# Optimization experiments

Measured on AMD Instinct MI355X. Metric: run time of the kernel, lower is better.

The kernel has to match this reference:

```python
import jax, jax.numpy as jnp
import numpy as np

N = 100_000
E = 1_250_000
D = 64
PAIRS = 3  # layer_num=3 -> 3 (SAGE, GIN) pairs
EPS = 1e-5


def _linear_init(key, fi, fo):
    lim = 1.0 / np.sqrt(fi)
    k1, k2 = jax.random.split(key)
    W = jax.random.uniform(k1, (fi, fo), minval=-lim, maxval=lim, dtype=jnp.float32)
    b = jax.random.uniform(k2, (fo,), minval=-lim, maxval=lim, dtype=jnp.float32)
    return W, b


def setup_inputs() -> dict:
    key = jax.random.key(0)
    ks = jax.random.split(key, 40)
    # graph
    src = jax.random.randint(ks[0], (E,), 0, N, dtype=jnp.int32)
    dst = jax.random.randint(ks[1], (E,), 0, N, dtype=jnp.int32)
    sign = (jax.random.randint(ks[2], (E,), 0, 2, dtype=jnp.int32) * 2 - 1)
    edge_index_s = jnp.stack([src, dst, sign], axis=1)  # [E,3]
    init_emb = jax.random.normal(ks[3], (N, D), dtype=jnp.float32)
    rate_b = jax.random.uniform(ks[4], (1,), dtype=jnp.float32)

    def stack_lin(kbase, fi, fo, n):
        Ws, bs = [], []
        for i in range(n):
            W, b = _linear_init(jax.random.fold_in(kbase, i), fi, fo)
            Ws.append(W); bs.append(b)
        return jnp.stack(Ws), jnp.stack(bs)

    sage_lin_W, sage_lin_b = stack_lin(ks[5], D, D, PAIRS)
    sage_norm_w = jnp.ones((PAIRS, D), jnp.float32)
    sage_norm_b = jnp.zeros((PAIRS, D), jnp.float32)
    rsW, rsB = stack_lin(ks[6], 1, D, PAIRS)   # rate_scale Linear(1,D)
    rbW, rbB = stack_lin(ks[7], 1, D, PAIRS)   # rate_bias Linear(1,D)
    sage_rs_w, sage_rs_b = rsW[:, 0, :], rsB   # [PAIRS,D]
    sage_rb_w, sage_rb_b = rbW[:, 0, :], rbB
    gin_W1, gin_b1 = stack_lin(ks[8], D, D, PAIRS)
    gin_W2, gin_b2 = stack_lin(ks[9], D, D, PAIRS)
    fuse_W, fuse_b = _linear_init(ks[10], 2 * PAIRS * D, D)
    ro_W1, ro_b1 = _linear_init(ks[11], D, 128)
    ro_W2, ro_b2 = _linear_init(ks[12], 128, 128)
    ro_W3, ro_b3 = _linear_init(ks[13], 128, 1)
    ro_ln1_g = jnp.ones((128,), jnp.float32); ro_ln1_b = jnp.zeros((128,), jnp.float32)
    ro_ln2_g = jnp.ones((128,), jnp.float32); ro_ln2_b = jnp.zeros((128,), jnp.float32)
    return dict(init_emb=init_emb, edge_index_s=edge_index_s, rate_b=rate_b,
                sage_lin_W=sage_lin_W, sage_lin_b=sage_lin_b,
                sage_norm_w=sage_norm_w, sage_norm_b=sage_norm_b,
                sage_rs_w=sage_rs_w, sage_rs_b=sage_rs_b,
                sage_rb_w=sage_rb_w, sage_rb_b=sage_rb_b,
                gin_W1=gin_W1, gin_b1=gin_b1, gin_W2=gin_W2, gin_b2=gin_b2,
                fuse_W=fuse_W, fuse_b=fuse_b,
                ro_W1=ro_W1, ro_b1=ro_b1, ro_ln1_g=ro_ln1_g, ro_ln1_b=ro_ln1_b,
                ro_W2=ro_W2, ro_b2=ro_b2, ro_ln2_g=ro_ln2_g, ro_ln2_b=ro_ln2_b,
                ro_W3=ro_W3, ro_b3=ro_b3)


def _graph_norm(x, w, b, rs_w, rs_b, rb_w, rb_b, rate):
    # batch stats over nodes (dim 0), biased variance
    mean = x.mean(0, keepdims=True)
    var = x.var(0, keepdims=True)
    x_norm = (x - mean) / jnp.sqrt(var + EPS)
    gamma = w + (rs_w * rate + rs_b)  # rate_scale(rate_b)
    beta = b + (rb_w * rate + rb_b)
    return x_norm * gamma + beta


def _layer_norm(v, g, b):
    m = v.mean(-1, keepdims=True)
    va = v.var(-1, keepdims=True)
    return (v - m) / jnp.sqrt(va + EPS) * g + b


def _forward(init_emb, edge_index_s, rate_b,
             sage_lin_W, sage_lin_b, sage_norm_w, sage_norm_b,
             sage_rs_w, sage_rs_b, sage_rb_w, sage_rb_b,
             gin_W1, gin_b1, gin_W2, gin_b2,
             fuse_W, fuse_b,
             ro_W1, ro_b1, ro_ln1_g, ro_ln1_b,
             ro_W2, ro_b2, ro_ln2_g, ro_ln2_b,
             ro_W3, ro_b3):
    n = init_emb.shape[0]
    src = edge_index_s[:, 0]
    dst = edge_index_s[:, 1]
    sign = edge_index_s[:, 2].astype(init_emb.dtype)
    rate = rate_b.reshape(())
    # degree including self-loop (for mean aggregation with fill_value=1 self loops)
    deg = jax.ops.segment_sum(jnp.ones_like(sign), dst, num_segments=n) + 1.0  # [n]
    gelu = lambda t: jax.nn.gelu(t, approximate=False)  # torch nn.GELU default = exact

    x = init_emb
    outputs = []
    for i in range(PAIRS):
        # --- StableEfficientEdgeSAGEConv (mean aggr, sign-scaled, self-loops, skip=Identity) ---
        xt = x @ sage_lin_W[i] + sage_lin_b[i]
        msg = sign[:, None] * xt[src]                                   # gather + sign scale
        agg = (jax.ops.segment_sum(msg, dst, num_segments=n) + xt) / deg[:, None]
        h = agg + x                                                     # skip (in==out -> Identity)
        h = _graph_norm(h, sage_norm_w[i], sage_norm_b[i],
                        sage_rs_w[i], sage_rs_b[i], sage_rb_w[i], sage_rb_b[i], rate)
        x = gelu(h)                                                     # dropout: eval mode (no-op)
        outputs.append(x)
        # --- GINConv (sum aggr, eps=0, no self-loops) mlp = Lin-GELU-Lin ---
        agg2 = jax.ops.segment_sum(x[src], dst, num_segments=n)
        z = x + agg2
        x = gelu(z @ gin_W1[i] + gin_b1[i]) @ gin_W2[i] + gin_b2[i]
        outputs.append(x)

    x_dense = jnp.concatenate(outputs, axis=1)          # [n, 6*D]
    x_final = x_dense @ fuse_W + fuse_b                 # [n, D]
    # readout MLP (2 hidden layers + head), eval-mode dropout
    hdd = jax.nn.relu(_layer_norm(x_final @ ro_W1 + ro_b1, ro_ln1_g, ro_ln1_b))
    hdd = jax.nn.relu(_layer_norm(hdd @ ro_W2 + ro_b2, ro_ln2_g, ro_ln2_b))
    prob = jax.nn.sigmoid(hdd @ ro_W3 + ro_b3)          # [n, 1]
    return x_final, prob


def reference(init_emb, edge_index_s, rate_b,
              sage_lin_W, sage_lin_b, sage_norm_w, sage_norm_b,
              sage_rs_w, sage_rs_b, sage_rb_w, sage_rb_b,
              gin_W1, gin_b1, gin_W2, gin_b2,
              fuse_W, fuse_b,
              ro_W1, ro_b1, ro_ln1_g, ro_ln1_b,
              ro_W2, ro_b2, ro_ln2_g, ro_ln2_b,
              ro_W3, ro_b3):
    return _forward(init_emb, edge_index_s, rate_b,
                    sage_lin_W, sage_lin_b, sage_norm_w, sage_norm_b,
                    sage_rs_w, sage_rs_b, sage_rb_w, sage_rb_b,
                    gin_W1, gin_b1, gin_W2, gin_b2,
                    fuse_W, fuse_b,
                    ro_W1, ro_b1, ro_ln1_g, ro_ln1_b,
                    ro_W2, ro_b2, ro_ln2_g, ro_ln2_b,
                    ro_W3, ro_b3)
```

## Files before the change

kernel.cpp:

```cpp
#include <hip/hip_runtime.h>
#include <hip/hip_bf16.h>
#include <math.h>


#define NBSHIFT 9
#define NBSIZE  512

__device__ __forceinline__ float gelu_f(float x) {
    return 0.5f * x * (1.0f + erff(x * 0.70710678118654752440f));
}
__device__ __forceinline__ unsigned short f2bf(float x) {
    __hip_bfloat16 h = __float2bfloat16(x);
    return *reinterpret_cast<unsigned short*>(&h);
}
__device__ __forceinline__ unsigned pack2bf(float a, float b) {
    return (unsigned)f2bf(a) | ((unsigned)f2bf(b) << 16);
}
__device__ __forceinline__ float bf2f(unsigned short u) {
    return __uint_as_float((unsigned)u << 16);
}

__global__ __launch_bounds__(256) void gemm64(
    const float* __restrict__ A,
    const float* __restrict__ Wa, const float* __restrict__ ba,
    unsigned short* __restrict__ Cb, int n)
{
    __shared__ __align__(16) float At[64][68];
    __shared__ __align__(16) float Ws[64][68];
    const int tid = threadIdx.x;
    const int tx = tid & 15, ty = tid >> 4;
    const int rowBase = blockIdx.x * 64;

    #pragma unroll
    for (int i = 0; i < 4; ++i) {
        int v  = tid + i * 256;
        int r  = v >> 4;
        int k4 = (v & 15) * 4;
        float4 a = make_float4(0.f, 0.f, 0.f, 0.f);
        int grow = rowBase + r;
        if (grow < n) a = *(const float4*)(A + (size_t)grow * 64 + k4);
        At[k4 + 0][r] = a.x; At[k4 + 1][r] = a.y;
        At[k4 + 2][r] = a.z; At[k4 + 3][r] = a.w;
        *(float4*)&Ws[r][k4] = *(const float4*)(Wa + r * 64 + k4);
    }
    __syncthreads();

    const int r0 = ty * 4, c0 = tx * 4;
    float acc[4][4];
    #pragma unroll
    for (int j = 0; j < 4; ++j) {
        float bv = ba[c0 + j];
        #pragma unroll
        for (int i = 0; i < 4; ++i) acc[i][j] = bv;
    }
    #pragma unroll 16
    for (int k = 0; k < 64; ++k) {
        float4 av = *(const float4*)&At[k][r0];
        float4 wv = *(const float4*)&Ws[k][c0];
        float a4[4] = {av.x, av.y, av.z, av.w};
        float w4[4] = {wv.x, wv.y, wv.z, wv.w};
        #pragma unroll
        for (int i = 0; i < 4; ++i)
            #pragma unroll
            for (int j = 0; j < 4; ++j)
                acc[i][j] = fmaf(a4[i], w4[j], acc[i][j]);
    }
    #pragma unroll
    for (int i = 0; i < 4; ++i) {
        int grow = rowBase + r0 + i;
        if (grow < n) {
            uint2 u;
            u.x = pack2bf(acc[i][0], acc[i][1]);
            u.y = pack2bf(acc[i][2], acc[i][3]);
            *(uint2*)(Cb + (size_t)grow * 64 + c0) = u;
        }
    }
}

template<bool FIRST>
__global__ __launch_bounds__(256) void act_fuse(
    const float* __restrict__ h,
    const float* __restrict__ colsum, const float* __restrict__ colsumsq,
    const float* __restrict__ nw, const float* __restrict__ nb,
    const float* __restrict__ rsw, const float* __restrict__ rsb,
    const float* __restrict__ rbw, const float* __restrict__ rbb,
    const float* __restrict__ rate_p, float inv_n,
    const float* __restrict__ Wf, const float* __restrict__ bf,
    unsigned short* __restrict__ xb, float* __restrict__ xfinal, int n)
{
    __shared__ __align__(16) float At[64][68];
    __shared__ __align__(16) float Ws[64][68];
    __shared__ float ab_s[128];
    const int tid = threadIdx.x;
    const int tx = tid & 15, ty = tid >> 4;
    const int rowBase = blockIdx.x * 64;

    if (tid < 64) {
        float mean = colsum[tid] * inv_n;
        float var  = colsumsq[tid] * inv_n - mean * mean;
        float rstd = rsqrtf(var + 1e-5f);
        float rate = rate_p[0];
        float gamma = nw[tid] + (rsw[tid] * rate + rsb[tid]);
        float beta  = nb[tid] + (rbw[tid] * rate + rbb[tid]);
        float a = rstd * gamma;
        ab_s[tid] = a;
        ab_s[64 + tid] = beta - mean * a;
    }
    __syncthreads();

    #pragma unroll
    for (int i = 0; i < 4; ++i) {
        int v  = tid + i * 256;
        int r  = v >> 4;
        int k4 = (v & 15) * 4;
        int grow = rowBase + r;
        float4 a = make_float4(0.f, 0.f, 0.f, 0.f);
        if (grow < n) {
            float4 hv = *(const float4*)(h + (size_t)grow * 64 + k4);
            a.x = gelu_f(fmaf(hv.x, ab_s[k4 + 0], ab_s[64 + k4 + 0]));
            a.y = gelu_f(fmaf(hv.y, ab_s[k4 + 1], ab_s[64 + k4 + 1]));
            a.z = gelu_f(fmaf(hv.z, ab_s[k4 + 2], ab_s[64 + k4 + 2]));
            a.w = gelu_f(fmaf(hv.w, ab_s[k4 + 3], ab_s[64 + k4 + 3]));
            uint2 u;
            u.x = pack2bf(a.x, a.y);
            u.y = pack2bf(a.z, a.w);
            *(uint2*)(xb + (size_t)grow * 64 + k4) = u;
        }
        At[k4 + 0][r] = a.x; At[k4 + 1][r] = a.y;
        At[k4 + 2][r] = a.z; At[k4 + 3][r] = a.w;
        *(float4*)&Ws[r][k4] = *(const float4*)(Wf + r * 64 + k4);
    }
    __syncthreads();

    const int r0 = ty * 4, c0 = tx * 4;
    float acc[4][4];
    if (FIRST) {
        #pragma unroll
        for (int j = 0; j < 4; ++j) {
            float bv = bf[c0 + j];
            #pragma unroll
            for (int i = 0; i < 4; ++i) acc[i][j] = bv;
        }
    } else {
        #pragma unroll
        for (int i = 0; i < 4; ++i)
            #pragma unroll
            for (int j = 0; j < 4; ++j) acc[i][j] = 0.f;
    }
    #pragma unroll 16
    for (int k = 0; k < 64; ++k) {
        float4 av = *(const float4*)&At[k][r0];
        float4 wv = *(const float4*)&Ws[k][c0];
        float a4[4] = {av.x, av.y, av.z, av.w};
        float w4[4] = {wv.x, wv.y, wv.z, wv.w};
        #pragma unroll
        for (int i = 0; i < 4; ++i)
            #pragma unroll
            for (int j = 0; j < 4; ++j)
                acc[i][j] = fmaf(a4[i], w4[j], acc[i][j]);
    }
    #pragma unroll
    for (int i = 0; i < 4; ++i) {
        int grow = rowBase + r0 + i;
        if (grow < n) {
            float4 r = make_float4(acc[i][0], acc[i][1], acc[i][2], acc[i][3]);
            float* cp = xfinal + (size_t)grow * 64 + c0;
            if (!FIRST) {
                float4 c = *(const float4*)cp;
                r.x += c.x; r.y += c.y; r.z += c.z; r.w += c.w;
            }
            *(float4*)cp = r;
        }
    }
}

template<bool NEXT>
__global__ __launch_bounds__(256) void gin_fuse(
    const float* __restrict__ z,
    const float* __restrict__ W1, const float* __restrict__ b1,
    const float* __restrict__ W2, const float* __restrict__ b2,
    const float* __restrict__ Wf,
    const float* __restrict__ Wn, const float* __restrict__ bn,
    float* __restrict__ xout, float* __restrict__ xfinal,
    unsigned short* __restrict__ bfout, int n)
{
    __shared__ __align__(16) float At[64][68];
    __shared__ __align__(16) float Ws[64][68];
    const int tid = threadIdx.x;
    const int tx = tid & 15, ty = tid >> 4;
    const int rowBase = blockIdx.x * 64;
    const int r0 = ty * 4, c0 = tx * 4;

    #pragma unroll
    for (int i = 0; i < 4; ++i) {
        int v  = tid + i * 256;
        int r  = v >> 4;
        int k4 = (v & 15) * 4;
        float4 a = make_float4(0.f, 0.f, 0.f, 0.f);
        int grow = rowBase + r;
        if (grow < n) a = *(const float4*)(z + (size_t)grow * 64 + k4);
        At[k4 + 0][r] = a.x; At[k4 + 1][r] = a.y;
        At[k4 + 2][r] = a.z; At[k4 + 3][r] = a.w;
        *(float4*)&Ws[r][k4] = *(const float4*)(W1 + r * 64 + k4);
    }
    __syncthreads();

    float acc[4][4];
    #pragma unroll
    for (int j = 0; j < 4; ++j) {
        float bv = b1[c0 + j];
        #pragma unroll
        for (int i = 0; i < 4; ++i) acc[i][j] = bv;
    }
    #pragma unroll 16
    for (int k = 0; k < 64; ++k) {
        float4 av = *(const float4*)&At[k][r0];
        float4 wv = *(const float4*)&Ws[k][c0];
        float a4[4] = {av.x, av.y, av.z, av.w};
        float w4[4] = {wv.x, wv.y, wv.z, wv.w};
        #pragma unroll
        for (int i = 0; i < 4; ++i)
            #pragma unroll
            for (int j = 0; j < 4; ++j)
                acc[i][j] = fmaf(a4[i], w4[j], acc[i][j]);
    }

    __syncthreads();
    #pragma unroll
    for (int i = 0; i < 4; ++i)
        #pragma unroll
        for (int j = 0; j < 4; ++j)
            At[c0 + j][r0 + i] = gelu_f(acc[i][j]);
    #pragma unroll
    for (int i = 0; i < 4; ++i) {
        int v = tid + i * 256;
        int k = v >> 4, c4 = (v & 15) * 4;
        *(float4*)&Ws[k][c4] = *(const float4*)(W2 + k * 64 + c4);
    }
    __syncthreads();
    float acc2[4][4];
    #pragma unroll
    for (int j = 0; j < 4; ++j) {
        float bv = b2[c0 + j];
        #pragma unroll
        for (int i = 0; i < 4; ++i) acc2[i][j] = bv;
    }
    #pragma unroll 16
    for (int k = 0; k < 64; ++k) {
        float4 av = *(const float4*)&At[k][r0];
        float4 wv = *(const float4*)&Ws[k][c0];
        float a4[4] = {av.x, av.y, av.z, av.w};
        float w4[4] = {wv.x, wv.y, wv.z, wv.w};
        #pragma unroll
        for (int i = 0; i < 4; ++i)
            #pragma unroll
            for (int j = 0; j < 4; ++j)
                acc2[i][j] = fmaf(a4[i], w4[j], acc2[i][j]);
    }
    #pragma unroll
    for (int i = 0; i < 4; ++i) {
        int grow = rowBase + r0 + i;
        if (grow < n)
            *(float4*)(xout + (size_t)grow * 64 + c0) =
                make_float4(acc2[i][0], acc2[i][1], acc2[i][2], acc2[i][3]);
    }

    __syncthreads();
    #pragma unroll
    for (int i = 0; i < 4; ++i)
        #pragma unroll
        for (int j = 0; j < 4; ++j)
            At[c0 + j][r0 + i] = acc2[i][j];
    #pragma unroll
    for (int i = 0; i < 4; ++i) {
        int v = tid + i * 256;
        int k = v >> 4, c4 = (v & 15) * 4;
        *(float4*)&Ws[k][c4] = *(const float4*)(Wf + k * 64 + c4);
    }
    __syncthreads();
    float acc3[4][4];
    #pragma unroll
    for (int i = 0; i < 4; ++i)
        #pragma unroll
        for (int j = 0; j < 4; ++j) acc3[i][j] = 0.f;
    #pragma unroll 16
    for (int k = 0; k < 64; ++k) {
        float4 av = *(const float4*)&At[k][r0];
        float4 wv = *(const float4*)&Ws[k][c0];
        float a4[4] = {av.x, av.y, av.z, av.w};
        float w4[4] = {wv.x, wv.y, wv.z, wv.w};
        #pragma unroll
        for (int i = 0; i < 4; ++i)
            #pragma unroll
            for (int j = 0; j < 4; ++j)
                acc3[i][j] = fmaf(a4[i], w4[j], acc3[i][j]);
    }
    #pragma unroll
    for (int i = 0; i < 4; ++i) {
        int grow = rowBase + r0 + i;
        if (grow < n) {
            float* cp = xfinal + (size_t)grow * 64 + c0;
            float4 c = *(const float4*)cp;
            c.x += acc3[i][0]; c.y += acc3[i][1];
            c.z += acc3[i][2]; c.w += acc3[i][3];
            *(float4*)cp = c;
        }
    }

    if (NEXT) {
        __syncthreads();
        #pragma unroll
        for (int i = 0; i < 4; ++i) {
            int v = tid + i * 256;
            int k = v >> 4, c4 = (v & 15) * 4;
            *(float4*)&Ws[k][c4] = *(const float4*)(Wn + k * 64 + c4);
        }
        __syncthreads();
        float acc4[4][4];
        #pragma unroll
        for (int j = 0; j < 4; ++j) {
            float bv = bn[c0 + j];
            #pragma unroll
            for (int i = 0; i < 4; ++i) acc4[i][j] = bv;
        }
        #pragma unroll 16
        for (int k = 0; k < 64; ++k) {
            float4 av = *(const float4*)&At[k][r0];
            float4 wv = *(const float4*)&Ws[k][c0];
            float a4[4] = {av.x, av.y, av.z, av.w};
            float w4[4] = {wv.x, wv.y, wv.z, wv.w};
            #pragma unroll
            for (int i = 0; i < 4; ++i)
                #pragma unroll
                for (int j = 0; j < 4; ++j)
                    acc4[i][j] = fmaf(a4[i], w4[j], acc4[i][j]);
        }
        #pragma unroll
        for (int i = 0; i < 4; ++i) {
            int grow = rowBase + r0 + i;
            if (grow < n) {
                uint2 u;
                u.x = pack2bf(acc4[i][0], acc4[i][1]);
                u.y = pack2bf(acc4[i][2], acc4[i][3]);
                *(uint2*)(bfout + (size_t)grow * 64 + c0) = u;
            }
        }
    }
}

__global__ void init_buckets(int* __restrict__ bucket_cursor, int Bn, int cap) {
    int t = threadIdx.x;
    if (t < Bn) bucket_cursor[t] = t * cap;
}

__global__ __launch_bounds__(256) void bucketA(
    const int* __restrict__ eidx, int* __restrict__ bucket_cursor,
    uint2* __restrict__ inter, int E)
{
    __shared__ int cnt[256], lo[256], cur[256], garr[256];
    __shared__ int tot_s;
    __shared__ uint2 stage[4096];
    const int tid = threadIdx.x;
    cnt[tid] = 0;
    __syncthreads();

    const int base = blockIdx.x * 4096;
    int pay[16], dfull[16];
    #pragma unroll
    for (int i = 0; i < 16; ++i) {
        int e = base + i * 256 + tid;
        dfull[i] = -1;
        if (e < E) {
            int s  = __builtin_nontemporal_load(eidx + e * 3 + 0);
            int d  = __builtin_nontemporal_load(eidx + e * 3 + 1);
            int sg = __builtin_nontemporal_load(eidx + e * 3 + 2);
            if (sg < 0) s |= 0x80000000;
            pay[i] = s;
            dfull[i] = d;
            atomicAdd(&cnt[d >> NBSHIFT], 1);
        }
    }
    __syncthreads();

    lo[tid] = cnt[tid];
    __syncthreads();
    for (int off = 1; off < 256; off <<= 1) {
        int t = (tid >= off) ? lo[tid - off] : 0;
        __syncthreads();
        lo[tid] += t;
        __syncthreads();
    }
    if (tid == 255) tot_s = lo[255];
    int excl = lo[tid] - cnt[tid];
    __syncthreads();
    lo[tid] = excl;
    cur[tid] = 0;
    if (cnt[tid] > 0) garr[tid] = atomicAdd(bucket_cursor + tid, cnt[tid]);
    __syncthreads();

    #pragma unroll
    for (int i = 0; i < 16; ++i) {
        if (dfull[i] >= 0) {
            int k = dfull[i] >> NBSHIFT;
            int r = atomicAdd(&cur[k], 1);
            stage[lo[k] + r] = make_uint2((unsigned)pay[i], (unsigned)dfull[i]);
        }
    }
    __syncthreads();

    const int tot = tot_s;
    for (int i = tid; i < tot; i += 256) {
        uint2 en = stage[i];
        int k = (int)(en.y >> NBSHIFT);
        inter[garr[k] + (i - lo[k])] = en;
    }
}

__global__ __launch_bounds__(256) void bucketB1(
    const uint2* __restrict__ inter, const int* __restrict__ bucket_cursor,
    int* __restrict__ deg_i, int cap, int n)
{
    __shared__ int cnt[NBSIZE];
    const int b = blockIdx.x, tid = threadIdx.x;
    cnt[tid] = 0; cnt[tid + 256] = 0;
    __syncthreads();
    const int base = b * cap;
    const int len = bucket_cursor[b] - base;
    for (int i = tid; i < len; i += 256)
        atomicAdd(&cnt[inter[base + i].y & (NBSIZE - 1)], 1);
    __syncthreads();
    const int nb0 = b << NBSHIFT;
    if (nb0 + tid < n)       deg_i[nb0 + tid]       = cnt[tid];
    if (nb0 + 256 + tid < n) deg_i[nb0 + 256 + tid] = cnt[256 + tid];
}

__global__ __launch_bounds__(256) void bucketB2(
    const uint2* __restrict__ inter, const int* __restrict__ bucket_cursor,
    const int* __restrict__ row_ptr, int* __restrict__ payload, int cap, int n)
{
    __shared__ int cur[NBSIZE];
    const int b = blockIdx.x, tid = threadIdx.x;
    const int nb0 = b << NBSHIFT;
    cur[tid]       = (nb0 + tid < n)       ? row_ptr[nb0 + tid]       : 0;
    cur[tid + 256] = (nb0 + 256 + tid < n) ? row_ptr[nb0 + 256 + tid] : 0;
    __syncthreads();
    const int base = b * cap;
    const int len = bucket_cursor[b] - base;
    for (int i = tid; i < len; i += 256) {
        uint2 en = inter[base + i];
        int pos = atomicAdd(&cur[en.y & (NBSIZE - 1)], 1);
        payload[pos] = (int)en.x;
    }
}

__global__ __launch_bounds__(256) void scan1(
    const int* __restrict__ deg_i, int* __restrict__ blocksum, int n, int chunk)
{
    int b = blockIdx.x;
    int lo = b * chunk, hi = min(lo + chunk, n);
    int s = 0;
    for (int i = lo + (int)threadIdx.x; i < hi; i += 256) s += deg_i[i];
    #pragma unroll
    for (int off = 32; off; off >>= 1) s += __shfl_xor(s, off, 64);
    __shared__ int ws[4];
    if ((threadIdx.x & 63) == 0) ws[threadIdx.x >> 6] = s;
    __syncthreads();
    if (threadIdx.x == 0) blocksum[b] = ws[0] + ws[1] + ws[2] + ws[3];
}

__global__ __launch_bounds__(256) void scan2(
    const int* __restrict__ blocksum, int* __restrict__ blockoff,
    int* __restrict__ row_ptr_n)
{
    int tid = threadIdx.x, lane = tid & 63, wid = tid >> 6;
    int orig = blocksum[tid];
    int v = orig;
    #pragma unroll
    for (int off = 1; off < 64; off <<= 1) {
        int t = __shfl_up(v, off, 64);
        if (lane >= off) v += t;
    }
    __shared__ int wt[4];
    if (lane == 63) wt[wid] = v;
    __syncthreads();
    int woff = 0;
    for (int w = 0; w < wid; ++w) woff += wt[w];
    blockoff[tid] = woff + v - orig;
    if (tid == 255) *row_ptr_n = woff + v;
}

__global__ __launch_bounds__(256) void scan3(
    const int* __restrict__ deg_i, const int* __restrict__ blockoff,
    int* __restrict__ row_ptr, float* __restrict__ rdeg, int n, int chunk)
{
    int b = blockIdx.x;
    int lo = b * chunk, hi = min(lo + chunk, n);
    int carry = blockoff[b];
    int tid = threadIdx.x, lane = tid & 63, wid = tid >> 6;
    __shared__ int wt[4];
    for (int base = lo; base < hi; base += 256) {
        int i = base + tid;
        int orig = (i < hi) ? deg_i[i] : 0;
        int v = orig;
        #pragma unroll
        for (int off = 1; off < 64; off <<= 1) {
            int t = __shfl_up(v, off, 64);
            if (lane >= off) v += t;
        }
        if (lane == 63) wt[wid] = v;
        __syncthreads();
        int woff = 0;
        for (int w = 0; w < wid; ++w) woff += wt[w];
        int tot = wt[0] + wt[1] + wt[2] + wt[3];
        int excl = carry + woff + (v - orig);
        if (i < hi) {
            row_ptr[i] = excl;
            rdeg[i]    = 1.0f / ((float)orig + 1.0f);
        }
        carry += tot;
        __syncthreads();
    }
}

__device__ __forceinline__ void accum8(float* a, uint4 u, float s) {
    a[0] = fmaf(__uint_as_float(u.x << 16),          s, a[0]);
    a[1] = fmaf(__uint_as_float(u.x & 0xffff0000u),  s, a[1]);
    a[2] = fmaf(__uint_as_float(u.y << 16),          s, a[2]);
    a[3] = fmaf(__uint_as_float(u.y & 0xffff0000u),  s, a[3]);
    a[4] = fmaf(__uint_as_float(u.z << 16),          s, a[4]);
    a[5] = fmaf(__uint_as_float(u.z & 0xffff0000u),  s, a[5]);
    a[6] = fmaf(__uint_as_float(u.w << 16),          s, a[6]);
    a[7] = fmaf(__uint_as_float(u.w & 0xffff0000u),  s, a[7]);
}

template<bool SAGE>
__global__ __launch_bounds__(256) void gather64(
    const int* __restrict__ row_ptr, const int* __restrict__ payload,
    const unsigned short* __restrict__ valb, const float* __restrict__ xprev,
    const float* __restrict__ rdeg, float* __restrict__ out,
    float* __restrict__ colsum, float* __restrict__ colsumsq, int n)
{
    const int tid  = threadIdx.x;
    const int lane = tid & 63;
    const int j8   = lane & 7;
    const int c0   = j8 * 8;
    const int wid  = tid >> 6;
    const int gg0  = (blockIdx.x * 256 + tid) >> 3;
    const int ng   = (gridDim.x * 256) >> 3;

    float st[8], st2[8];
    if (SAGE) {
        #pragma unroll
        for (int k = 0; k < 8; ++k) { st[k] = 0.f; st2[k] = 0.f; }
    }

    for (int node = gg0; __any(node < n); node += ng) {
        const bool active  = node < n;
        const int  selfrow = active ? node : 0;
        const int  beg     = active ? row_ptr[node]     : 0;
        const int  end     = active ? row_ptr[node + 1] : 0;

        int t = (end - beg + 3) >> 2;
        t = max(t, __shfl_xor(t, 8, 64));
        t = max(t, __shfl_xor(t, 16, 64));
        t = max(t, __shfl_xor(t, 32, 64));

        float a[8];
        #pragma unroll
        for (int k = 0; k < 8; ++k) a[k] = 0.f;

        int p0 = (beg + 0 < end) ? payload[beg + 0] : 0;
        int p1 = (beg + 1 < end) ? payload[beg + 1] : 0;
        int p2 = (beg + 2 < end) ? payload[beg + 2] : 0;
        int p3 = (beg + 3 < end) ? payload[beg + 3] : 0;

        for (int it = 0; it < t; ++it) {
            const int i0 = beg + (it << 2);
            const bool w0 = i0 + 0 < end, w1 = i0 + 1 < end;
            const bool w2 = i0 + 2 < end, w3 = i0 + 3 < end;
            const int q0 = p0, q1 = p1, q2 = p2, q3 = p3;

            const int r0 = w0 ? (q0 & 0x7fffffff) : selfrow;
            const int r1 = w1 ? (q1 & 0x7fffffff) : selfrow;
            const int r2 = w2 ? (q2 & 0x7fffffff) : selfrow;
            const int r3 = w3 ? (q3 & 0x7fffffff) : selfrow;
            uint4 u0 = *(const uint4*)(valb + (size_t)r0 * 64 + c0);
            uint4 u1 = *(const uint4*)(valb + (size_t)r1 * 64 + c0);
            uint4 u2 = *(const uint4*)(valb + (size_t)r2 * 64 + c0);
            uint4 u3 = *(const uint4*)(valb + (size_t)r3 * 64 + c0);

            const int nb = i0 + 4;
            p0 = (nb + 0 < end) ? payload[nb + 0] : 0;
            p1 = (nb + 1 < end) ? payload[nb + 1] : 0;
            p2 = (nb + 2 < end) ? payload[nb + 2] : 0;
            p3 = (nb + 3 < end) ? payload[nb + 3] : 0;

            const float s0 = w0 ? ((SAGE && q0 < 0) ? -1.f : 1.f) : 0.f;
            const float s1 = w1 ? ((SAGE && q1 < 0) ? -1.f : 1.f) : 0.f;
            const float s2 = w2 ? ((SAGE && q2 < 0) ? -1.f : 1.f) : 0.f;
            const float s3 = w3 ? ((SAGE && q3 < 0) ? -1.f : 1.f) : 0.f;
            accum8(a, u0, s0);
            accum8(a, u1, s1);
            accum8(a, u2, s2);
            accum8(a, u3, s3);
        }

        uint4 us = *(const uint4*)(valb + (size_t)selfrow * 64 + c0);
        accum8(a, us, 1.f);

        if (SAGE) {
            const float rd = active ? rdeg[node] : 0.f;
            float4 xp0 = *(const float4*)(xprev + (size_t)selfrow * 64 + c0);
            float4 xp1 = *(const float4*)(xprev + (size_t)selfrow * 64 + c0 + 4);
            float xp[8] = {xp0.x, xp0.y, xp0.z, xp0.w,
                           xp1.x, xp1.y, xp1.z, xp1.w};
            float h[8];
            #pragma unroll
            for (int k = 0; k < 8; ++k) h[k] = fmaf(a[k], rd, xp[k]);
            if (active) {
                #pragma unroll
                for (int k = 0; k < 8; ++k) {
                    st[k]  += h[k];
                    st2[k] += h[k] * h[k];
                }
                *(float4*)(out + (size_t)node * 64 + c0) =
                    make_float4(h[0], h[1], h[2], h[3]);
                *(float4*)(out + (size_t)node * 64 + c0 + 4) =
                    make_float4(h[4], h[5], h[6], h[7]);
            }
        } else {
            if (active) {
                *(float4*)(out + (size_t)node * 64 + c0) =
                    make_float4(a[0], a[1], a[2], a[3]);
                *(float4*)(out + (size_t)node * 64 + c0 + 4) =
                    make_float4(a[4], a[5], a[6], a[7]);
            }
        }
    }

    if (SAGE) {
        #pragma unroll
        for (int k = 0; k < 8; ++k) {
            st[k]  += __shfl_xor(st[k], 8, 64);
            st[k]  += __shfl_xor(st[k], 16, 64);
            st[k]  += __shfl_xor(st[k], 32, 64);
            st2[k] += __shfl_xor(st2[k], 8, 64);
            st2[k] += __shfl_xor(st2[k], 16, 64);
            st2[k] += __shfl_xor(st2[k], 32, 64);
        }
        __shared__ float sh[2][4][64];
        if (lane < 8) {
            #pragma unroll
            for (int k = 0; k < 8; ++k) {
                sh[0][wid][c0 + k] = st[k];
                sh[1][wid][c0 + k] = st2[k];
            }
        }
        __syncthreads();
        if (tid < 64) {
            float a_ = sh[0][0][tid] + sh[0][1][tid] + sh[0][2][tid] + sh[0][3][tid];
            float b_ = sh[1][0][tid] + sh[1][1][tid] + sh[1][2][tid] + sh[1][3][tid];
            atomicAdd(colsum + tid, a_);
            atomicAdd(colsumsq + tid, b_);
        }
    }
}

__global__ __launch_bounds__(256) void readout1(
    const float* __restrict__ xf, const float* __restrict__ W1,
    const float* __restrict__ b1, const float* __restrict__ g1,
    const float* __restrict__ bt1, float* __restrict__ H, int n)
{
    __shared__ __align__(16) float At[64][68];
    __shared__ __align__(16) float Ws[64][132];
    const int tid = threadIdx.x;
    const int tx = tid & 15, ty = tid >> 4;
    const int rowBase = blockIdx.x * 64;

    #pragma unroll
    for (int i = 0; i < 4; ++i) {
        int v = tid + i * 256;
        int r = v >> 4, k4 = (v & 15) * 4;
        float4 a = make_float4(0.f, 0.f, 0.f, 0.f);
        int grow = rowBase + r;
        if (grow < n) a = *(const float4*)(xf + (size_t)grow * 64 + k4);
        At[k4 + 0][r] = a.x; At[k4 + 1][r] = a.y;
        At[k4 + 2][r] = a.z; At[k4 + 3][r] = a.w;
    }
    #pragma unroll
    for (int i = 0; i < 8; ++i) {
        int v = tid + i * 256;
        int k = v >> 5, c4 = (v & 31) * 4;
        *(float4*)&Ws[k][c4] = *(const float4*)(W1 + k * 128 + c4);
    }
    __syncthreads();

    const int r0 = ty * 4, c0 = tx * 8;
    float acc[4][8];
    #pragma unroll
    for (int j = 0; j < 8; ++j) {
        float bv = b1[c0 + j];
        #pragma unroll
        for (int i = 0; i < 4; ++i) acc[i][j] = bv;
    }
    #pragma unroll 8
    for (int k = 0; k < 64; ++k) {
        float4 av = *(const float4*)&At[k][r0];
        float4 w0 = *(const float4*)&Ws[k][c0];
        float4 w1v = *(const float4*)&Ws[k][c0 + 4];
        float a4[4] = {av.x, av.y, av.z, av.w};
        float w8[8] = {w0.x, w0.y, w0.z, w0.w, w1v.x, w1v.y, w1v.z, w1v.w};
        #pragma unroll
        for (int i = 0; i < 4; ++i)
            #pragma unroll
            for (int j = 0; j < 8; ++j)
                acc[i][j] = fmaf(a4[i], w8[j], acc[i][j]);
    }

    float gj[8], bj[8];
    #pragma unroll
    for (int j = 0; j < 8; ++j) { gj[j] = g1[c0 + j]; bj[j] = bt1[c0 + j]; }
    #pragma unroll
    for (int i = 0; i < 4; ++i) {
        int grow = rowBase + r0 + i;
        float s = 0.f, s2 = 0.f;
        #pragma unroll
        for (int j = 0; j < 8; ++j) { s += acc[i][j]; s2 += acc[i][j] * acc[i][j]; }
        #pragma unroll
        for (int off = 8; off; off >>= 1) {
            s  += __shfl_xor(s, off, 16);
            s2 += __shfl_xor(s2, off, 16);
        }
        float mean = s * (1.f / 128.f);
        float var  = s2 * (1.f / 128.f) - mean * mean;
        float rstd = rsqrtf(var + 1e-5f);
        float o[8];
        #pragma unroll
        for (int j = 0; j < 8; ++j)
            o[j] = fmaxf(fmaf((acc[i][j] - mean) * rstd, gj[j], bj[j]), 0.f);
        if (grow < n) {
            *(float4*)(H + (size_t)grow * 128 + c0)     = make_float4(o[0], o[1], o[2], o[3]);
            *(float4*)(H + (size_t)grow * 128 + c0 + 4) = make_float4(o[4], o[5], o[6], o[7]);
        }
    }
}

__global__ __launch_bounds__(256) void readout2(
    const float* __restrict__ H, const float* __restrict__ W2,
    const float* __restrict__ b2, const float* __restrict__ g2,
    const float* __restrict__ bt2, const float* __restrict__ W3,
    const float* __restrict__ b3, float* __restrict__ prob, int n)
{
    __shared__ __align__(16) float Ht[64][68];
    __shared__ __align__(16) float Ws[64][132];
    const int tid = threadIdx.x;
    const int tx = tid & 15, ty = tid >> 4;
    const int rowBase = blockIdx.x * 64;
    const int r0 = ty * 4, c0 = tx * 8;

    float acc[4][8];
    #pragma unroll
    for (int j = 0; j < 8; ++j) {
        float bv = b2[c0 + j];
        #pragma unroll
        for (int i = 0; i < 4; ++i) acc[i][j] = bv;
    }

    for (int kc = 0; kc < 2; ++kc) {
        if (kc) __syncthreads();
        #pragma unroll
        for (int i = 0; i < 4; ++i) {
            int v = tid + i * 256;
            int r = v >> 4, k4 = (v & 15) * 4;
            float4 a = make_float4(0.f, 0.f, 0.f, 0.f);
            int grow = rowBase + r;
            if (grow < n) a = *(const float4*)(H + (size_t)grow * 128 + kc * 64 + k4);
            Ht[k4 + 0][r] = a.x; Ht[k4 + 1][r] = a.y;
            Ht[k4 + 2][r] = a.z; Ht[k4 + 3][r] = a.w;
        }
        #pragma unroll
        for (int i = 0; i < 8; ++i) {
            int v = tid + i * 256;
            int k = v >> 5, c4 = (v & 31) * 4;
            *(float4*)&Ws[k][c4] = *(const float4*)(W2 + (kc * 64 + k) * 128 + c4);
        }
        __syncthreads();
        #pragma unroll 8
        for (int k = 0; k < 64; ++k) {
            float4 av = *(const float4*)&Ht[k][r0];
            float4 w0 = *(const float4*)&Ws[k][c0];
            float4 w1v = *(const float4*)&Ws[k][c0 + 4];
            float a4[4] = {av.x, av.y, av.z, av.w};
            float w8[8] = {w0.x, w0.y, w0.z, w0.w, w1v.x, w1v.y, w1v.z, w1v.w};
            #pragma unroll
            for (int i = 0; i < 4; ++i)
                #pragma unroll
                for (int j = 0; j < 8; ++j)
                    acc[i][j] = fmaf(a4[i], w8[j], acc[i][j]);
        }
    }

    float gj[8], bj[8], w3[8];
    #pragma unroll
    for (int j = 0; j < 8; ++j) {
        gj[j] = g2[c0 + j]; bj[j] = bt2[c0 + j]; w3[j] = W3[c0 + j];
    }
    const float bias3 = b3[0];
    #pragma unroll
    for (int i = 0; i < 4; ++i) {
        int grow = rowBase + r0 + i;
        float s = 0.f, s2 = 0.f;
        #pragma unroll
        for (int j = 0; j < 8; ++j) { s += acc[i][j]; s2 += acc[i][j] * acc[i][j]; }
        #pragma unroll
        for (int off = 8; off; off >>= 1) {
            s  += __shfl_xor(s, off, 16);
            s2 += __shfl_xor(s2, off, 16);
        }
        float mean = s * (1.f / 128.f);
        float var  = s2 * (1.f / 128.f) - mean * mean;
        float rstd = rsqrtf(var + 1e-5f);
        float d = 0.f;
        #pragma unroll
        for (int j = 0; j < 8; ++j) {
            float v = fmaxf(fmaf((acc[i][j] - mean) * rstd, gj[j], bj[j]), 0.f);
            d = fmaf(v, w3[j], d);
        }
        #pragma unroll
        for (int off = 8; off; off >>= 1) d += __shfl_xor(d, off, 16);
        if (tx == 0 && grow < n)
            prob[grow] = 1.f / (1.f + expf(-(d + bias3)));
    }
}

extern "C" void kernel_launch(void* const* d_in, const int* in_sizes, int n_in,
                              void* d_out, int out_size, void* d_ws, size_t ws_size,
                              hipStream_t stream)
{
    const float* init_emb = (const float*)d_in[0];
    const int*   eidx     = (const int*)d_in[1];
    const float* rate_b   = (const float*)d_in[2];
    const float* sage_W   = (const float*)d_in[3];
    const float* sage_b   = (const float*)d_in[4];
    const float* norm_w   = (const float*)d_in[5];
    const float* norm_b   = (const float*)d_in[6];
    const float* rs_w     = (const float*)d_in[7];
    const float* rs_b     = (const float*)d_in[8];
    const float* rb_w     = (const float*)d_in[9];
    const float* rb_b     = (const float*)d_in[10];
    const float* gin_W1   = (const float*)d_in[11];
    const float* gin_b1   = (const float*)d_in[12];
    const float* gin_W2   = (const float*)d_in[13];
    const float* gin_b2   = (const float*)d_in[14];
    const float* fuse_W   = (const float*)d_in[15];
    const float* fuse_b   = (const float*)d_in[16];
    const float* ro_W1    = (const float*)d_in[17];
    const float* ro_b1    = (const float*)d_in[18];
    const float* ln1_g    = (const float*)d_in[19];
    const float* ln1_b    = (const float*)d_in[20];
    const float* ro_W2    = (const float*)d_in[21];
    const float* ro_b2    = (const float*)d_in[22];
    const float* ln2_g    = (const float*)d_in[23];
    const float* ln2_b    = (const float*)d_in[24];
    const float* ro_W3    = (const float*)d_in[25];
    const float* ro_b3    = (const float*)d_in[26];

    const int N = in_sizes[0] / 64;
    const int E = in_sizes[1] / 3;
    const size_t nf = (size_t)N * 64;

    float* bufA  = (float*)d_ws;
    float* bufB  = bufA + nf;
    float* bufC  = bufB + nf;
    unsigned short* bfbuf = (unsigned short*)(bufC + nf);
    float* rdeg  = (float*)(bfbuf + nf);
    float* stats = rdeg + N;
    int*   row_ptr  = (int*)(stats + 3 * 256);
    int*   deg_i    = row_ptr + (N + 1);
    int*   blocksum = deg_i + N;
    int*   blockoff = blocksum + 256;
    int*   bucket_cursor = blockoff + 256;
    int*   payload  = bucket_cursor + 256;
    uint2* inter    = (uint2*)bufC;

    float* xfinal = (float*)d_out;
    float* prob   = xfinal + nf;
    float* H      = bufA;

    const int gemm_blocks = (N + 63) / 64;
    const int gather_blocks = 2048;
    const int chunk  = (N + 255) / 256;
    const float inv_n = 1.0f / (float)N;

    const int Bn   = (N + NBSIZE - 1) / NBSIZE;
    const int meanb = (E + Bn - 1) / Bn;
    const int cap  = meanb + meanb / 8 + 64;
    const int ablocks = (E + 4095) / 4096;

    hipMemsetAsync(stats, 0, 3 * 256 * sizeof(float), stream);
    init_buckets<<<1, 256, 0, stream>>>(bucket_cursor, Bn, cap);
    bucketA<<<ablocks, 256, 0, stream>>>(eidx, bucket_cursor, inter, E);
    bucketB1<<<Bn, 256, 0, stream>>>(inter, bucket_cursor, deg_i, cap, N);
    scan1<<<256, 256, 0, stream>>>(deg_i, blocksum, N, chunk);
    scan2<<<1, 256, 0, stream>>>(blocksum, blockoff, row_ptr + N);
    scan3<<<256, 256, 0, stream>>>(deg_i, blockoff, row_ptr, rdeg, N, chunk);
    bucketB2<<<Bn, 256, 0, stream>>>(inter, bucket_cursor, row_ptr, payload, cap, N);

    for (int p = 0; p < 3; ++p) {
        const float* Xp = (p == 0) ? init_emb : (p == 1 ? (const float*)bufB : (const float*)bufC);
        float* B2p = (p == 1) ? bufC : bufB;
        float* cs = stats + p * 256;

        if (p == 0)
            gemm64<<<gemm_blocks, 256, 0, stream>>>(
                Xp, sage_W, sage_b, bfbuf, N);
        gather64<true><<<gather_blocks, 256, 0, stream>>>(
            row_ptr, payload, bfbuf, Xp, rdeg, B2p, cs, cs + 64, N);
        if (p == 0)
            act_fuse<true><<<gemm_blocks, 256, 0, stream>>>(
                B2p, cs, cs + 64,
                norm_w + p * 64, norm_b + p * 64, rs_w + p * 64, rs_b + p * 64,
                rb_w + p * 64, rb_b + p * 64, rate_b, inv_n,
                fuse_W, fuse_b, bfbuf, xfinal, N);
        else
            act_fuse<false><<<gemm_blocks, 256, 0, stream>>>(
                B2p, cs, cs + 64,
                norm_w + p * 64, norm_b + p * 64, rs_w + p * 64, rs_b + p * 64,
                rb_w + p * 64, rb_b + p * 64, rate_b, inv_n,
                fuse_W + (2 * p) * 4096, nullptr, bfbuf, xfinal, N);
        gather64<false><<<gather_blocks, 256, 0, stream>>>(
            row_ptr, payload, bfbuf, nullptr, nullptr, B2p, nullptr, nullptr, N);
        if (p < 2)
            gin_fuse<true><<<gemm_blocks, 256, 0, stream>>>(
                B2p, gin_W1 + p * 4096, gin_b1 + p * 64,
                gin_W2 + p * 4096, gin_b2 + p * 64,
                fuse_W + (2 * p + 1) * 4096,
                sage_W + (p + 1) * 4096, sage_b + (p + 1) * 64,
                B2p, xfinal, bfbuf, N);
        else
            gin_fuse<false><<<gemm_blocks, 256, 0, stream>>>(
                B2p, gin_W1 + p * 4096, gin_b1 + p * 64,
                gin_W2 + p * 4096, gin_b2 + p * 64,
                fuse_W + (2 * p + 1) * 4096,
                nullptr, nullptr, B2p, xfinal, nullptr, N);
    }

    readout1<<<gemm_blocks, 256, 0, stream>>>(
        xfinal, ro_W1, ro_b1, ln1_g, ln1_b, H, N);
    readout2<<<gemm_blocks, 256, 0, stream>>>(
        H, ro_W2, ro_b2, ln2_g, ln2_b, ro_W3, ro_b3, prob, N);
}
```

Baseline: 822.7 us.

## Vectorize transposed LDS tile stores and use nontemporal loads/stores in gather

```diff
diff --git a/kernel.cpp b/kernel.cpp
--- a/kernel.cpp
+++ b/kernel.cpp
@@ -5,6 +5,8 @@
 
 #define NBSHIFT 9
 #define NBSIZE  512
+
+typedef float vf4 __attribute__((ext_vector_type(4)));
 
 __device__ __forceinline__ float gelu_f(float x) {
     return 0.5f * x * (1.0f + erff(x * 0.70710678118654752440f));
@@ -30,18 +32,30 @@
     const int tid = threadIdx.x;
     const int tx = tid & 15, ty = tid >> 4;
     const int rowBase = blockIdx.x * 64;
-
-    #pragma unroll
-    for (int i = 0; i < 4; ++i) {
-        int v  = tid + i * 256;
-        int r  = v >> 4;
-        int k4 = (v & 15) * 4;
-        float4 a = make_float4(0.f, 0.f, 0.f, 0.f);
-        int grow = rowBase + r;
-        if (grow < n) a = *(const float4*)(A + (size_t)grow * 64 + k4);
-        At[k4 + 0][r] = a.x; At[k4 + 1][r] = a.y;
-        At[k4 + 2][r] = a.z; At[k4 + 3][r] = a.w;
-        *(float4*)&Ws[r][k4] = *(const float4*)(Wa + r * 64 + k4);
+    const int ty4 = ty * 4;
+
+    {
+        float4 R[4];
+        #pragma unroll
+        for (int i = 0; i < 4; ++i) {
+            int grow = rowBase + ty4 + i;
+            R[i] = make_float4(0.f, 0.f, 0.f, 0.f);
+            if (grow < n) R[i] = *(const float4*)(A + (size_t)grow * 64 + tx * 4);
+        }
+        #pragma unroll
+        for (int j = 0; j < 4; ++j) {
+            float4 c = make_float4(((const float*)&R[0])[j],
+                                   ((const float*)&R[1])[j],
+                                   ((const float*)&R[2])[j],
+                                   ((const float*)&R[3])[j]);
+            *(float4*)&At[tx * 4 + j][ty4] = c;
+        }
+        #pragma unroll
+        for (int i = 0; i < 4; ++i) {
+            int v = tid + i * 256;
+            int r = v >> 4, k4 = (v & 15) * 4;
+            *(float4*)&Ws[r][k4] = *(const float4*)(Wa + r * 64 + k4);
+        }
     }
     __syncthreads();
 
@@ -94,6 +108,7 @@
     const int tid = threadIdx.x;
     const int tx = tid & 15, ty = tid >> 4;
     const int rowBase = blockIdx.x * 64;
+    const int ty4 = ty * 4;
 
     if (tid < 64) {
         float mean = colsum[tid] * inv_n;
@@ -108,27 +123,43 @@
     }
     __syncthreads();
 
-    #pragma unroll
-    for (int i = 0; i < 4; ++i) {
-        int v  = tid + i * 256;
-        int r  = v >> 4;
-        int k4 = (v & 15) * 4;
-        int grow = rowBase + r;
-        float4 a = make_float4(0.f, 0.f, 0.f, 0.f);
-        if (grow < n) {
-            float4 hv = *(const float4*)(h + (size_t)grow * 64 + k4);
-            a.x = gelu_f(fmaf(hv.x, ab_s[k4 + 0], ab_s[64 + k4 + 0]));
-            a.y = gelu_f(fmaf(hv.y, ab_s[k4 + 1], ab_s[64 + k4 + 1]));
-            a.z = gelu_f(fmaf(hv.z, ab_s[k4 + 2], ab_s[64 + k4 + 2]));
-            a.w = gelu_f(fmaf(hv.w, ab_s[k4 + 3], ab_s[64 + k4 + 3]));
-            uint2 u;
-            u.x = pack2bf(a.x, a.y);
-            u.y = pack2bf(a.z, a.w);
-            *(uint2*)(xb + (size_t)grow * 64 + k4) = u;
-        }
-        At[k4 + 0][r] = a.x; At[k4 + 1][r] = a.y;
-        At[k4 + 2][r] = a.z; At[k4 + 3][r] = a.w;
-        *(float4*)&Ws[r][k4] = *(const float4*)(Wf + r * 64 + k4);
+    {
+        const float s0 = ab_s[tx * 4 + 0], s1 = ab_s[tx * 4 + 1];
+        const float s2 = ab_s[tx * 4 + 2], s3 = ab_s[tx * 4 + 3];
+        const float o0 = ab_s[64 + tx * 4 + 0], o1 = ab_s[64 + tx * 4 + 1];
+        const float o2 = ab_s[64 + tx * 4 + 2], o3 = ab_s[64 + tx * 4 + 3];
+        float4 R[4];
+        #pragma unroll
+        for (int i = 0; i < 4; ++i) {
+            int grow = rowBase + ty4 + i;
+            float4 a = make_float4(0.f, 0.f, 0.f, 0.f);
+            if (grow < n) {
+                float4 hv = *(const float4*)(h + (size_t)grow * 64 + tx * 4);
+                a.x = gelu_f(fmaf(hv.x, s0, o0));
+                a.y = gelu_f(fmaf(hv.y, s1, o1));
+                a.z = gelu_f(fmaf(hv.z, s2, o2));
+                a.w = gelu_f(fmaf(hv.w, s3, o3));
+                uint2 u;
+                u.x = pack2bf(a.x, a.y);
+                u.y = pack2bf(a.z, a.w);
+                *(uint2*)(xb + (size_t)grow * 64 + tx * 4) = u;
+            }
+            R[i] = a;
+        }
+        #pragma unroll
+        for (int j = 0; j < 4; ++j) {
+            float4 c = make_float4(((const float*)&R[0])[j],
+                                   ((const float*)&R[1])[j],
+                                   ((const float*)&R[2])[j],
+                                   ((const float*)&R[3])[j]);
+            *(float4*)&At[tx * 4 + j][ty4] = c;
+        }
+        #pragma unroll
+        for (int i = 0; i < 4; ++i) {
+            int v = tid + i * 256;
+            int r = v >> 4, k4 = (v & 15) * 4;
+            *(float4*)&Ws[r][k4] = *(const float4*)(Wf + r * 64 + k4);
+        }
     }
     __syncthreads();
 
@@ -190,18 +221,30 @@
     const int tx = tid & 15, ty = tid >> 4;
     const int rowBase = blockIdx.x * 64;
     const int r0 = ty * 4, c0 = tx * 4;
-
-    #pragma unroll
-    for (int i = 0; i < 4; ++i) {
-        int v  = tid + i * 256;
-        int r  = v >> 4;
-        int k4 = (v & 15) * 4;
-        float4 a = make_float4(0.f, 0.f, 0.f, 0.f);
-        int grow = rowBase + r;
-        if (grow < n) a = *(const float4*)(z + (size_t)grow * 64 + k4);
-        At[k4 + 0][r] = a.x; At[k4 + 1][r] = a.y;
-        At[k4 + 2][r] = a.z; At[k4 + 3][r] = a.w;
-        *(float4*)&Ws[r][k4] = *(const float4*)(W1 + r * 64 + k4);
+    const int ty4 = ty * 4;
+
+    {
+        float4 R[4];
+        #pragma unroll
+        for (int i = 0; i < 4; ++i) {
+            int grow = rowBase + ty4 + i;
+            R[i] = make_float4(0.f, 0.f, 0.f, 0.f);
+            if (grow < n) R[i] = *(const float4*)(z + (size_t)grow * 64 + tx * 4);
+        }
+        #pragma unroll
+        for (int j = 0; j < 4; ++j) {
+            float4 c = make_float4(((const float*)&R[0])[j],
+                                   ((const float*)&R[1])[j],
+                                   ((const float*)&R[2])[j],
+                                   ((const float*)&R[3])[j]);
+            *(float4*)&At[tx * 4 + j][ty4] = c;
+        }
+        #pragma unroll
+        for (int i = 0; i < 4; ++i) {
+            int v = tid + i * 256;
+            int r = v >> 4, k4 = (v & 15) * 4;
+            *(float4*)&Ws[r][k4] = *(const float4*)(W1 + r * 64 + k4);
+        }
     }
     __syncthreads();
 
@@ -227,10 +270,11 @@
 
     __syncthreads();
     #pragma unroll
-    for (int i = 0; i < 4; ++i)
-        #pragma unroll
-        for (int j = 0; j < 4; ++j)
-            At[c0 + j][r0 + i] = gelu_f(acc[i][j]);
+    for (int j = 0; j < 4; ++j) {
+        float4 c = make_float4(gelu_f(acc[0][j]), gelu_f(acc[1][j]),
+                               gelu_f(acc[2][j]), gelu_f(acc[3][j]));
+        *(float4*)&At[c0 + j][r0] = c;
+    }
     #pragma unroll
     for (int i = 0; i < 4; ++i) {
         int v = tid + i * 256;
@@ -267,10 +311,10 @@
 
     __syncthreads();
     #pragma unroll
-    for (int i = 0; i < 4; ++i)
-        #pragma unroll
-        for (int j = 0; j < 4; ++j)
-            At[c0 + j][r0 + i] = acc2[i][j];
+    for (int j = 0; j < 4; ++j) {
+        float4 c = make_float4(acc2[0][j], acc2[1][j], acc2[2][j], acc2[3][j]);
+        *(float4*)&At[c0 + j][r0] = c;
+    }
     #pragma unroll
     for (int i = 0; i < 4; ++i) {
         int v = tid + i * 256;
@@ -569,10 +613,10 @@
         #pragma unroll
         for (int k = 0; k < 8; ++k) a[k] = 0.f;
 
-        int p0 = (beg + 0 < end) ? payload[beg + 0] : 0;
-        int p1 = (beg + 1 < end) ? payload[beg + 1] : 0;
-        int p2 = (beg + 2 < end) ? payload[beg + 2] : 0;
-        int p3 = (beg + 3 < end) ? payload[beg + 3] : 0;
+        int p0 = (beg + 0 < end) ? __builtin_nontemporal_load(payload + beg + 0) : 0;
+        int p1 = (beg + 1 < end) ? __builtin_nontemporal_load(payload + beg + 1) : 0;
+        int p2 = (beg + 2 < end) ? __builtin_nontemporal_load(payload + beg + 2) : 0;
+        int p3 = (beg + 3 < end) ? __builtin_nontemporal_load(payload + beg + 3) : 0;
 
         for (int it = 0; it < t; ++it) {
             const int i0 = beg + (it << 2);
@@ -590,10 +634,10 @@
             uint4 u3 = *(const uint4*)(valb + (size_t)r3 * 64 + c0);
 
             const int nb = i0 + 4;
-            p0 = (nb + 0 < end) ? payload[nb + 0] : 0;
-            p1 = (nb + 1 < end) ? payload[nb + 1] : 0;
-            p2 = (nb + 2 < end) ? payload[nb + 2] : 0;
-            p3 = (nb + 3 < end) ? payload[nb + 3] : 0;
+            p0 = (nb + 0 < end) ? __builtin_nontemporal_load(payload + nb + 0) : 0;
+            p1 = (nb + 1 < end) ? __builtin_nontemporal_load(payload + nb + 1) : 0;
+            p2 = (nb + 2 < end) ? __builtin_nontemporal_load(payload + nb + 2) : 0;
+            p3 = (nb + 3 < end) ? __builtin_nontemporal_load(payload + nb + 3) : 0;
 
             const float s0 = w0 ? ((SAGE && q0 < 0) ? -1.f : 1.f) : 0.f;
             const float s1 = w1 ? ((SAGE && q1 < 0) ? -1.f : 1.f) : 0.f;
@@ -609,9 +653,11 @@
         accum8(a, us, 1.f);
 
         if (SAGE) {
-            const float rd = active ? rdeg[node] : 0.f;
-            float4 xp0 = *(const float4*)(xprev + (size_t)selfrow * 64 + c0);
-            float4 xp1 = *(const float4*)(xprev + (size_t)selfrow * 64 + c0 + 4);
+            const float rd = active ? __builtin_nontemporal_load(rdeg + node) : 0.f;
+            vf4 xp0 = __builtin_nontemporal_load(
+                (const vf4*)(xprev + (size_t)selfrow * 64 + c0));
+            vf4 xp1 = __builtin_nontemporal_load(
+                (const vf4*)(xprev + (size_t)selfrow * 64 + c0 + 4));
             float xp[8] = {xp0.x, xp0.y, xp0.z, xp0.w,
                            xp1.x, xp1.y, xp1.z, xp1.w};
             float h[8];
@@ -623,17 +669,17 @@
                     st[k]  += h[k];
                     st2[k] += h[k] * h[k];
                 }
-                *(float4*)(out + (size_t)node * 64 + c0) =
-                    make_float4(h[0], h[1], h[2], h[3]);
-                *(float4*)(out + (size_t)node * 64 + c0 + 4) =
-                    make_float4(h[4], h[5], h[6], h[7]);
+                vf4 o0 = {h[0], h[1], h[2], h[3]};
+                vf4 o1 = {h[4], h[5], h[6], h[7]};
+                __builtin_nontemporal_store(o0, (vf4*)(out + (size_t)node * 64 + c0));
+                __builtin_nontemporal_store(o1, (vf4*)(out + (size_t)node * 64 + c0 + 4));
             }
         } else {
             if (active) {
-                *(float4*)(out + (size_t)node * 64 + c0) =
-                    make_float4(a[0], a[1], a[2], a[3]);
-                *(float4*)(out + (size_t)node * 64 + c0 + 4) =
-                    make_float4(a[4], a[5], a[6], a[7]);
+                vf4 o0 = {a[0], a[1], a[2], a[3]};
+                vf4 o1 = {a[4], a[5], a[6], a[7]};
+                __builtin_nontemporal_store(o0, (vf4*)(out + (size_t)node * 64 + c0));
+                __builtin_nontemporal_store(o1, (vf4*)(out + (size_t)node * 64 + c0 + 4));
             }
         }
     }
@@ -676,16 +722,24 @@
     const int tid = threadIdx.x;
     const int tx = tid & 15, ty = tid >> 4;
     const int rowBase = blockIdx.x * 64;
-
-    #pragma unroll
-    for (int i = 0; i < 4; ++i) {
-        int v = tid + i * 256;
-        int r = v >> 4, k4 = (v & 15) * 4;
-        float4 a = make_float4(0.f, 0.f, 0.f, 0.f);
-        int grow = rowBase + r;
-        if (grow < n) a = *(const float4*)(xf + (size_t)grow * 64 + k4);
-        At[k4 + 0][r] = a.x; At[k4 + 1][r] = a.y;
-        At[k4 + 2][r] = a.z; At[k4 + 3][r] = a.w;
+    const int ty4 = ty * 4;
+
+    {
+        float4 R[4];
+        #pragma unroll
+        for (int i = 0; i < 4; ++i) {
+            int grow = rowBase + ty4 + i;
+            R[i] = make_float4(0.f, 0.f, 0.f, 0.f);
+            if (grow < n) R[i] = *(const float4*)(xf + (size_t)grow * 64 + tx * 4);
+        }
+        #pragma unroll
+        for (int j = 0; j < 4; ++j) {
+            float4 c = make_float4(((const float*)&R[0])[j],
+                                   ((const float*)&R[1])[j],
+                                   ((const float*)&R[2])[j],
+                                   ((const float*)&R[3])[j]);
+            *(float4*)&At[tx * 4 + j][ty4] = c;
+        }
     }
     #pragma unroll
     for (int i = 0; i < 8; ++i) {
@@ -757,6 +811,7 @@
     const int tx = tid & 15, ty = tid >> 4;
     const int rowBase = blockIdx.x * 64;
     const int r0 = ty * 4, c0 = tx * 8;
+    const int ty4 = ty * 4;
 
     float acc[4][8];
     #pragma unroll
@@ -768,15 +823,23 @@
 
     for (int kc = 0; kc < 2; ++kc) {
         if (kc) __syncthreads();
-        #pragma unroll
-        for (int i = 0; i < 4; ++i) {
-            int v = tid + i * 256;
-            int r = v >> 4, k4 = (v & 15) * 4;
-            float4 a = make_float4(0.f, 0.f, 0.f, 0.f);
-            int grow = rowBase + r;
-            if (grow < n) a = *(const float4*)(H + (size_t)grow * 128 + kc * 64 + k4);
-            Ht[k4 + 0][r] = a.x; Ht[k4 + 1][r] = a.y;
-            Ht[k4 + 2][r] = a.z; Ht[k4 + 3][r] = a.w;
+        {
+            float4 R[4];
+            #pragma unroll
+            for (int i = 0; i < 4; ++i) {
+                int grow = rowBase + ty4 + i;
+                R[i] = make_float4(0.f, 0.f, 0.f, 0.f);
+                if (grow < n)
+                    R[i] = *(const float4*)(H + (size_t)grow * 128 + kc * 64 + tx * 4);
+            }
+            #pragma unroll
+            for (int j = 0; j < 4; ++j) {
+                float4 c = make_float4(((const float*)&R[0])[j],
+                                       ((const float*)&R[1])[j],
+                                       ((const float*)&R[2])[j],
+                                       ((const float*)&R[3])[j]);
+                *(float4*)&Ht[tx * 4 + j][ty4] = c;
+            }
         }
         #pragma unroll
         for (int i = 0; i < 8; ++i) {
```

Result: slower. 854.2 us (+3.8%).
